# Kernel tuning notes

Hardware: AMD Instinct MI355X
Metric: run time of the kernel (lower is better)

The kernel has to match this reference:

```python
import jax, jax.numpy as jnp
import numpy as np

L, M, K = 13, 12, 5
ODD_KS = tuple(range(1, K + 1, 2))  # (1, 3, 5) -> n_odd_order = 3
NK = len(ODD_KS)


def setup_inputs() -> dict:
    key = jax.random.key(0)
    k1, k2, k3, k4 = jax.random.split(key, 4)
    B, T = 16, 8192
    x = jax.random.normal(k1, (B, T, 2), dtype=jnp.float32)
    h_0 = jnp.zeros((B, 16), dtype=jnp.float32)  # unused by forward (API compat)
    A_kl = jax.random.normal(k2, (L, NK), dtype=jnp.float32) * 0.1
    B_klm = jax.random.normal(k3, (L, M, NK), dtype=jnp.float32) * 0.1
    C_klm = jax.random.normal(k4, (L, M, NK), dtype=jnp.float32) * 0.1
    return {"x": x, "h_0": h_0, "A_kl": A_kl, "B_klm": B_klm, "C_klm": C_klm}


def _gmp_forward(x, A_kl, B_klm, C_klm):
    # x: [B, T, 2] real/imag -> complex signal
    Bsz, T, _ = x.shape
    xc = jax.lax.complex(x[..., 0], x[..., 1])  # [B, T]

    # Circular window indices (equivalent to torch cat+unfold in the original).
    t = jnp.arange(T)[:, None, None]
    l = jnp.arange(L)[None, :, None]
    m = jnp.arange(M + 1)[None, None, :]
    # 2nd term pads with the LAST (L+M-1) samples at the front -> index shift back
    idx2 = (t + l + m - (L + M - 1)) % T  # [T, L, M+1]
    # 3rd term pads with the FIRST (L+M-1) samples at the end -> forward wrap
    idx3 = (t + l + m) % T                # [T, L, M+1]

    x2 = xc[:, idx2]  # [B, T, L, M+1] complex
    x3 = xc[:, idx3]  # [B, T, L, M+1] complex
    # First-term window x[t-(L-1)+l] equals the m=M element of the 2nd-term window.
    x1 = x2[..., -1]  # [B, T, L]

    # --- term 1: sum_{l,k} A[l,k] * x1 * |x1|^k ---
    a1 = jnp.abs(x1)                                        # [B,T,L]
    p1 = jnp.stack([a1 ** k for k in ODD_KS], axis=-1)       # [B,T,L,NK] real
    c1 = jnp.einsum('btlk,lk->btl', p1, A_kl)                # real coefficient
    term1 = jnp.sum(x1 * c1, axis=-1)                        # [B,T] complex

    # --- term 2: sum_{l,m,k} B[l,m,k] * x2[...,M] * |x2[...,m]|^k ---
    a2 = jnp.abs(x2[..., :-1])                               # [B,T,L,M]
    p2 = jnp.stack([a2 ** k for k in ODD_KS], axis=-1)       # [B,T,L,M,NK]
    c2 = jnp.einsum('btlmk,lmk->btl', p2, B_klm)             # sum over m,k too
    term2 = jnp.sum(x1 * c2, axis=-1)                        # multiplier is x2[...,-1]==x1

    # --- term 3: same structure with forward-lag windows and C ---
    x3_last = x3[..., -1]                                    # [B,T,L]
    a3 = jnp.abs(x3[..., :-1])                               # [B,T,L,M]
    p3 = jnp.stack([a3 ** k for k in ODD_KS], axis=-1)       # [B,T,L,M,NK]
    c3 = jnp.einsum('btlmk,lmk->btl', p3, C_klm)
    term3 = jnp.sum(x3_last * c3, axis=-1)

    s = term1 + term2 + term3                                # [B,T] complex
    return jnp.stack([jnp.real(s), jnp.imag(s)], axis=-1)    # [B,T,2] float32


def reference(x, h_0, A_kl, B_klm, C_klm):
    # h_0 is accepted but unused, matching the torch module.
    return _gmp_forward(x, A_kl, B_klm, C_klm)
```

## Files before the change

### kernel.cpp

```cpp
#include <hip/hip_runtime.h>
#include <math.h>

#define LL    13
#define MM    12
#define NKK   3
#define OUTS  64
#define BLOCK 256
#define HALO  24
#define WIN   (OUTS + 2*HALO)
#define NWB   (25 * LL)
#define NWC   (24 * LL)

__shared__ float4 sP[WIN];
__shared__ float2 sZ[WIN];
__shared__ float4 sWB[NWB];
__shared__ float4 sWC[NWC];
__shared__ float2 sAcc[4][OUTS];

template<int D0, int D1, int POFS>
__device__ __forceinline__ void conv_half(const float4* __restrict__ sW,
                                          int o, float c[LL])
{
    #pragma unroll
    for (int d = D0; d < D1; ++d) {
        const float4 p = sP[o + POFS + d];
        #pragma unroll
        for (int l = 0; l < LL; ++l) {
            const int m = d - l;
            if (m >= 0 && m <= MM) {
                const float4 w = sW[d * LL + l];
                c[l] += w.x * p.x + w.y * p.y + w.z * p.z;
            }
        }
    }
}

__global__ __launch_bounds__(BLOCK)
void gmp_kernel(const float* __restrict__ x,
                const float* __restrict__ Ac,
                const float* __restrict__ Bc,
                const float* __restrict__ Cc,
                float* __restrict__ out,
                int T, int tilesPerB)
{
    const int tid = threadIdx.x;
    const int b   = blockIdx.x / tilesPerB;
    const int t0  = (blockIdx.x % tilesPerB) * OUTS;

    const float* xb = x + (size_t)b * T * 2;

    if (tid < WIN) {
        int t = t0 - HALO + tid;
        if (t < 0)  t += T;
        if (t >= T) t -= T;
        const float2 z = *(const float2*)(xb + 2 * t);
        float a2 = z.x * z.x + z.y * z.y;
        float a  = sqrtf(a2);
        sZ[tid] = z;
        sP[tid] = make_float4(a, a * a2, a * a2 * a2, 0.0f);
    }

    for (int idx = tid; idx < NWB; idx += BLOCK) {
        const int d = idx / LL;
        const int l = idx - d * LL;
        const int m = d - l;
        float4 w = make_float4(0.f, 0.f, 0.f, 0.f);
        if (m >= 0 && m <= MM) {
            const float* s = (m == MM) ? (Ac + l * NKK)
                                       : (Bc + (l * MM + m) * NKK);
            w = make_float4(s[0], s[1], s[2], 0.f);
        }
        sWB[idx] = w;
    }
    for (int idx = tid; idx < NWC; idx += BLOCK) {
        const int d = idx / LL;
        const int l = idx - d * LL;
        const int m = d - l;
        float4 w = make_float4(0.f, 0.f, 0.f, 0.f);
        if (m >= 0 && m < MM) {
            const float* s = Cc + (l * MM + m) * NKK;
            w = make_float4(s[0], s[1], s[2], 0.f);
        }
        sWC[idx] = w;
    }
    __syncthreads();

    const int o    = tid & 63;
    const int role = tid >> 6;

    float c[LL];
    #pragma unroll
    for (int l = 0; l < LL; ++l) c[l] = 0.f;

    if      (role == 0) conv_half< 0, 13,  0>(sWB, o, c);
    else if (role == 1) conv_half<13, 25,  0>(sWB, o, c);
    else if (role == 2) conv_half< 0, 12, 24>(sWC, o, c);
    else                conv_half<12, 24, 24>(sWC, o, c);

    const int zofs = (role < 2) ? 12 : 36;
    float sr = 0.f, si = 0.f;
    #pragma unroll
    for (int l = 0; l < LL; ++l) {
        const float2 z = sZ[o + l + zofs];
        sr += z.x * c[l];
        si += z.y * c[l];
    }
    sAcc[role][o] = make_float2(sr, si);
    __syncthreads();

    if (tid < OUTS) {
        const float2 a0 = sAcc[0][tid];
        const float2 a1 = sAcc[1][tid];
        const float2 a2 = sAcc[2][tid];
        const float2 a3 = sAcc[3][tid];
        const int t = t0 + tid;
        if (t < T) {
            float2* op = (float2*)(out + ((size_t)b * T + t) * 2);
            *op = make_float2(a0.x + a1.x + a2.x + a3.x,
                              a0.y + a1.y + a2.y + a3.y);
        }
    }
}

extern "C" void kernel_launch(void* const* d_in, const int* in_sizes, int n_in,
                              void* d_out, int out_size, void* d_ws, size_t ws_size,
                              hipStream_t stream)
{
    const float* x  = (const float*)d_in[0];
    const float* Ac = (const float*)d_in[2];
    const float* Bc = (const float*)d_in[3];
    const float* Cc = (const float*)d_in[4];
    float* out = (float*)d_out;

    const int Bsz = in_sizes[1] / 16;
    const int T   = in_sizes[0] / (2 * Bsz);
    const int tilesPerB = (T + OUTS - 1) / OUTS;

    dim3 grid(Bsz * tilesPerB);
    dim3 block(BLOCK);
    gmp_kernel<<<grid, block, 0, stream>>>(x, Ac, Bc, Cc, out, T, tilesPerB);
}
```

Measured before the change: 78.12 us.

## Register-block four outputs per thread with larger tiles and split power layout

Each block now computes 512 outputs instead of 64. Each thread computes four adjacent outputs, holding a sliding window of power values in registers, so every weight loaded from shared memory is reused four times. The power and signal arrays are stored interleaved by residue mod 4 so that the per-thread window loads stay contiguous. The B and C terms are split across two thread halves instead of four quarter-roles. This raises register pressure considerably, and the grid shrinks to 256 blocks, which may underfill the GPU.

```diff
diff --git a/kernel.cpp b/kernel.cpp
--- a/kernel.cpp
+++ b/kernel.cpp
@@ -4,36 +4,13 @@
 #define LL    13
 #define MM    12
 #define NKK   3
-#define OUTS  64
+#define OUTS  512
 #define BLOCK 256
 #define HALO  24
 #define WIN   (OUTS + 2*HALO)
+#define WIN4  (WIN/4)
 #define NWB   (25 * LL)
 #define NWC   (24 * LL)
-
-__shared__ float4 sP[WIN];
-__shared__ float2 sZ[WIN];
-__shared__ float4 sWB[NWB];
-__shared__ float4 sWC[NWC];
-__shared__ float2 sAcc[4][OUTS];
-
-template<int D0, int D1, int POFS>
-__device__ __forceinline__ void conv_half(const float4* __restrict__ sW,
-                                          int o, float c[LL])
-{
-    #pragma unroll
-    for (int d = D0; d < D1; ++d) {
-        const float4 p = sP[o + POFS + d];
-        #pragma unroll
-        for (int l = 0; l < LL; ++l) {
-            const int m = d - l;
-            if (m >= 0 && m <= MM) {
-                const float4 w = sW[d * LL + l];
-                c[l] += w.x * p.x + w.y * p.y + w.z * p.z;
-            }
-        }
-    }
-}
 
 __global__ __launch_bounds__(BLOCK)
 void gmp_kernel(const float* __restrict__ x,
@@ -43,21 +20,29 @@
                 float* __restrict__ out,
                 int T, int tilesPerB)
 {
+    __shared__ float2 sPa[4][WIN4];
+    __shared__ float  sPb[4][WIN4];
+    __shared__ float2 sZ4[4][WIN4];
+    __shared__ float4 sWB[NWB];
+    __shared__ float4 sWC[NWC];
+    __shared__ float2 sAcc[2][OUTS];
+
     const int tid = threadIdx.x;
     const int b   = blockIdx.x / tilesPerB;
     const int t0  = (blockIdx.x % tilesPerB) * OUTS;
 
     const float* xb = x + (size_t)b * T * 2;
 
-    if (tid < WIN) {
-        int t = t0 - HALO + tid;
+    for (int j = tid; j < WIN; j += BLOCK) {
+        int t = t0 - HALO + j;
         if (t < 0)  t += T;
         if (t >= T) t -= T;
         const float2 z = *(const float2*)(xb + 2 * t);
         float a2 = z.x * z.x + z.y * z.y;
         float a  = sqrtf(a2);
-        sZ[tid] = z;
-        sP[tid] = make_float4(a, a * a2, a * a2 * a2, 0.0f);
+        sZ4[j & 3][j >> 2] = z;
+        sPa[j & 3][j >> 2] = make_float2(a, a * a2);
+        sPb[j & 3][j >> 2] = a * a2 * a2;
     }
 
     for (int idx = tid; idx < NWB; idx += BLOCK) {
@@ -85,39 +70,108 @@
     }
     __syncthreads();
 
-    const int o    = tid & 63;
-    const int role = tid >> 6;
+    const int g     = tid & 127;
+    const int roleC = tid >> 7;
+    const int o0    = g * 4;
 
-    float c[LL];
+    float cc[4][LL];
     #pragma unroll
-    for (int l = 0; l < LL; ++l) c[l] = 0.f;
+    for (int r = 0; r < 4; ++r)
+        #pragma unroll
+        for (int l = 0; l < LL; ++l) cc[r][l] = 0.f;
 
-    if      (role == 0) conv_half< 0, 13,  0>(sWB, o, c);
-    else if (role == 1) conv_half<13, 25,  0>(sWB, o, c);
-    else if (role == 2) conv_half< 0, 12, 24>(sWC, o, c);
-    else                conv_half<12, 24, 24>(sWC, o, c);
+    float sr[4], si[4];
 
-    const int zofs = (role < 2) ? 12 : 36;
-    float sr = 0.f, si = 0.f;
+    if (roleC == 0) {
+        float2 pa[28]; float pb[28];
+        #pragma unroll
+        for (int k = 0; k < 28; ++k) {
+            pa[k] = sPa[k & 3][g + (k >> 2)];
+            pb[k] = sPb[k & 3][g + (k >> 2)];
+        }
+        #pragma unroll
+        for (int d = 0; d < 25; ++d) {
+            #pragma unroll
+            for (int l = 0; l < LL; ++l) {
+                const int m = d - l;
+                if (m >= 0 && m <= MM) {
+                    const float4 w = sWB[d * LL + l];
+                    #pragma unroll
+                    for (int r = 0; r < 4; ++r) {
+                        cc[r][l] += w.x * pa[d + r].x
+                                  + w.y * pa[d + r].y
+                                  + w.z * pb[d + r];
+                    }
+                }
+            }
+        }
+        float2 zw[16];
+        #pragma unroll
+        for (int k = 0; k < 16; ++k)
+            zw[k] = sZ4[k & 3][g + 3 + (k >> 2)];
+        #pragma unroll
+        for (int r = 0; r < 4; ++r) {
+            sr[r] = 0.f; si[r] = 0.f;
+            #pragma unroll
+            for (int l = 0; l < LL; ++l) {
+                const float2 z = zw[r + l];
+                sr[r] += z.x * cc[r][l];
+                si[r] += z.y * cc[r][l];
+            }
+        }
+    } else {
+        float2 pa[27]; float pb[27];
+        #pragma unroll
+        for (int k = 0; k < 27; ++k) {
+            pa[k] = sPa[k & 3][g + 6 + (k >> 2)];
+            pb[k] = sPb[k & 3][g + 6 + (k >> 2)];
+        }
+        #pragma unroll
+        for (int d = 0; d < 24; ++d) {
+            #pragma unroll
+            for (int l = 0; l < LL; ++l) {
+                const int m = d - l;
+                if (m >= 0 && m < MM) {
+                    const float4 w = sWC[d * LL + l];
+                    #pragma unroll
+                    for (int r = 0; r < 4; ++r) {
+                        cc[r][l] += w.x * pa[d + r].x
+                                  + w.y * pa[d + r].y
+                                  + w.z * pb[d + r];
+                    }
+                }
+            }
+        }
+        float2 zw[16];
+        #pragma unroll
+        for (int k = 0; k < 16; ++k)
+            zw[k] = sZ4[k & 3][g + 9 + (k >> 2)];
+        #pragma unroll
+        for (int r = 0; r < 4; ++r) {
+            sr[r] = 0.f; si[r] = 0.f;
+            #pragma unroll
+            for (int l = 0; l < LL; ++l) {
+                const float2 z = zw[r + l];
+                sr[r] += z.x * cc[r][l];
+                si[r] += z.y * cc[r][l];
+            }
+        }
+    }
+
     #pragma unroll
-    for (int l = 0; l < LL; ++l) {
-        const float2 z = sZ[o + l + zofs];
-        sr += z.x * c[l];
-        si += z.y * c[l];
-    }
-    sAcc[role][o] = make_float2(sr, si);
+    for (int r = 0; r < 4; ++r)
+        sAcc[roleC][o0 + r] = make_float2(sr[r], si[r]);
     __syncthreads();
 
-    if (tid < OUTS) {
-        const float2 a0 = sAcc[0][tid];
-        const float2 a1 = sAcc[1][tid];
-        const float2 a2 = sAcc[2][tid];
-        const float2 a3 = sAcc[3][tid];
-        const int t = t0 + tid;
+    #pragma unroll
+    for (int s = 0; s < 2; ++s) {
+        const int j = tid + s * BLOCK;
+        const float2 a0 = sAcc[0][j];
+        const float2 a1 = sAcc[1][j];
+        const int t = t0 + j;
         if (t < T) {
             float2* op = (float2*)(out + ((size_t)b * T + t) * 2);
-            *op = make_float2(a0.x + a1.x + a2.x + a3.x,
-                              a0.y + a1.y + a2.y + a3.y);
+            *op = make_float2(a0.x + a1.x, a0.y + a1.y);
         }
     }
 }
```

Measured after the change: 78.42 us. About the same (+0.4%).

## Register-block two outputs per thread with a larger tile and split SoA shared layout

Applied to the files above, without the earlier changes.

Each thread now computes two adjacent outputs and reuses every shared-memory weight load for both. Input magnitudes are cached in registers, and the work is split into two roles (B-term and C-term) instead of four. The tile grows to 256 outputs per block, which cuts the halo and weight-staging overhead per output. Shared arrays are split by even/odd index into float2/float arrays to avoid bank conflicts. The cost is higher register pressure (two 13-wide accumulators plus about 26 cached inputs), which is bounded by launch_bounds(256,2), and fewer blocks in the grid.

```diff
diff --git a/kernel.cpp b/kernel.cpp
--- a/kernel.cpp
+++ b/kernel.cpp
@@ -4,38 +4,15 @@
 #define LL    13
 #define MM    12
 #define NKK   3
-#define OUTS  64
+#define OUTS  256
 #define BLOCK 256
 #define HALO  24
 #define WIN   (OUTS + 2*HALO)
+#define WIN2  (WIN/2)
 #define NWB   (25 * LL)
 #define NWC   (24 * LL)
 
-__shared__ float4 sP[WIN];
-__shared__ float2 sZ[WIN];
-__shared__ float4 sWB[NWB];
-__shared__ float4 sWC[NWC];
-__shared__ float2 sAcc[4][OUTS];
-
-template<int D0, int D1, int POFS>
-__device__ __forceinline__ void conv_half(const float4* __restrict__ sW,
-                                          int o, float c[LL])
-{
-    #pragma unroll
-    for (int d = D0; d < D1; ++d) {
-        const float4 p = sP[o + POFS + d];
-        #pragma unroll
-        for (int l = 0; l < LL; ++l) {
-            const int m = d - l;
-            if (m >= 0 && m <= MM) {
-                const float4 w = sW[d * LL + l];
-                c[l] += w.x * p.x + w.y * p.y + w.z * p.z;
-            }
-        }
-    }
-}
-
-__global__ __launch_bounds__(BLOCK)
+__global__ __launch_bounds__(BLOCK, 2)
 void gmp_kernel(const float* __restrict__ x,
                 const float* __restrict__ Ac,
                 const float* __restrict__ Bc,
@@ -43,21 +20,29 @@
                 float* __restrict__ out,
                 int T, int tilesPerB)
 {
+    __shared__ float2 sPa[2][WIN2];
+    __shared__ float  sPb[2][WIN2];
+    __shared__ float2 sZ2[2][WIN2];
+    __shared__ float4 sWB[NWB];
+    __shared__ float4 sWC[NWC];
+    __shared__ float4 sAcc[2][BLOCK/2];
+
     const int tid = threadIdx.x;
     const int b   = blockIdx.x / tilesPerB;
     const int t0  = (blockIdx.x % tilesPerB) * OUTS;
 
     const float* xb = x + (size_t)b * T * 2;
 
-    if (tid < WIN) {
-        int t = t0 - HALO + tid;
+    for (int j = tid; j < WIN; j += BLOCK) {
+        int t = t0 - HALO + j;
         if (t < 0)  t += T;
         if (t >= T) t -= T;
         const float2 z = *(const float2*)(xb + 2 * t);
         float a2 = z.x * z.x + z.y * z.y;
         float a  = sqrtf(a2);
-        sZ[tid] = z;
-        sP[tid] = make_float4(a, a * a2, a * a2 * a2, 0.0f);
+        sZ2[j & 1][j >> 1] = z;
+        sPa[j & 1][j >> 1] = make_float2(a, a * a2);
+        sPb[j & 1][j >> 1] = a * a2 * a2;
     }
 
     for (int idx = tid; idx < NWB; idx += BLOCK) {
@@ -85,39 +70,87 @@
     }
     __syncthreads();
 
-    const int o    = tid & 63;
-    const int role = tid >> 6;
+    const int g    = tid & 127;
+    const int role = tid >> 7;
 
-    float c[LL];
+    float cc[2][LL];
     #pragma unroll
-    for (int l = 0; l < LL; ++l) c[l] = 0.f;
+    for (int l = 0; l < LL; ++l) { cc[0][l] = 0.f; cc[1][l] = 0.f; }
 
-    if      (role == 0) conv_half< 0, 13,  0>(sWB, o, c);
-    else if (role == 1) conv_half<13, 25,  0>(sWB, o, c);
-    else if (role == 2) conv_half< 0, 12, 24>(sWC, o, c);
-    else                conv_half<12, 24, 24>(sWC, o, c);
+    float sr0, si0, sr1, si1;
 
-    const int zofs = (role < 2) ? 12 : 36;
-    float sr = 0.f, si = 0.f;
-    #pragma unroll
-    for (int l = 0; l < LL; ++l) {
-        const float2 z = sZ[o + l + zofs];
-        sr += z.x * c[l];
-        si += z.y * c[l];
+    if (role == 0) {
+        float2 pa[26]; float pb[26];
+        #pragma unroll
+        for (int k = 0; k < 26; ++k) {
+            pa[k] = sPa[k & 1][g + (k >> 1)];
+            pb[k] = sPb[k & 1][g + (k >> 1)];
+        }
+        #pragma unroll
+        for (int d = 0; d < 25; ++d) {
+            #pragma unroll
+            for (int l = 0; l < LL; ++l) {
+                const int m = d - l;
+                if (m >= 0 && m <= MM) {
+                    const float4 w = sWB[d * LL + l];
+                    cc[0][l] += w.x * pa[d  ].x + w.y * pa[d  ].y + w.z * pb[d  ];
+                    cc[1][l] += w.x * pa[d+1].x + w.y * pa[d+1].y + w.z * pb[d+1];
+                }
+            }
+        }
+        float2 zw[14];
+        #pragma unroll
+        for (int k = 0; k < 14; ++k)
+            zw[k] = sZ2[k & 1][g + 6 + (k >> 1)];
+        sr0 = si0 = sr1 = si1 = 0.f;
+        #pragma unroll
+        for (int l = 0; l < LL; ++l) {
+            sr0 += zw[l    ].x * cc[0][l];  si0 += zw[l    ].y * cc[0][l];
+            sr1 += zw[l + 1].x * cc[1][l];  si1 += zw[l + 1].y * cc[1][l];
+        }
+    } else {
+        float2 pa[25]; float pb[25];
+        #pragma unroll
+        for (int k = 0; k < 25; ++k) {
+            pa[k] = sPa[k & 1][g + 12 + (k >> 1)];
+            pb[k] = sPb[k & 1][g + 12 + (k >> 1)];
+        }
+        #pragma unroll
+        for (int d = 0; d < 24; ++d) {
+            #pragma unroll
+            for (int l = 0; l < LL; ++l) {
+                const int m = d - l;
+                if (m >= 0 && m < MM) {
+                    const float4 w = sWC[d * LL + l];
+                    cc[0][l] += w.x * pa[d  ].x + w.y * pa[d  ].y + w.z * pb[d  ];
+                    cc[1][l] += w.x * pa[d+1].x + w.y * pa[d+1].y + w.z * pb[d+1];
+                }
+            }
+        }
+        float2 zw[14];
+        #pragma unroll
+        for (int k = 0; k < 14; ++k)
+            zw[k] = sZ2[k & 1][g + 18 + (k >> 1)];
+        sr0 = si0 = sr1 = si1 = 0.f;
+        #pragma unroll
+        for (int l = 0; l < LL; ++l) {
+            sr0 += zw[l    ].x * cc[0][l];  si0 += zw[l    ].y * cc[0][l];
+            sr1 += zw[l + 1].x * cc[1][l];  si1 += zw[l + 1].y * cc[1][l];
+        }
     }
-    sAcc[role][o] = make_float2(sr, si);
+
+    sAcc[role][g] = make_float4(sr0, si0, sr1, si1);
     __syncthreads();
 
-    if (tid < OUTS) {
-        const float2 a0 = sAcc[0][tid];
-        const float2 a1 = sAcc[1][tid];
-        const float2 a2 = sAcc[2][tid];
-        const float2 a3 = sAcc[3][tid];
+    {
+        const float2* p0 = (const float2*)&sAcc[0][0];
+        const float2* p1 = (const float2*)&sAcc[1][0];
+        const float2 a0 = p0[tid];
+        const float2 a1 = p1[tid];
         const int t = t0 + tid;
         if (t < T) {
             float2* op = (float2*)(out + ((size_t)b * T + t) * 2);
-            *op = make_float2(a0.x + a1.x + a2.x + a3.x,
-                              a0.y + a1.y + a2.y + a3.y);
+            *op = make_float2(a0.x + a1.x, a0.y + a1.y);
         }
     }
 }
```

New measurement: 70.13 us. 10.2% less time.
